# Kernel optimization log

Measured on AMD Instinct MI355X. Metric: run time of the kernel, lower is better.

The kernel has to match this reference:

```python
import jax, jax.numpy as jnp
import numpy as np

B, C_IN, C_OUT, H, K = 256, 64, 128, 1039, 6  # batch, in_ch, out_ch, num_hexagons, max_neighbors


def _make_neighbors(rng, num_hex, max_n):
    # valid neighbor indices first, -1 padding at the end (matches torch init)
    nb = np.full((num_hex, max_n), -1, dtype=np.int64)
    counts = rng.integers(3, max_n + 1, size=num_hex)
    for i in range(num_hex):
        nb[i, :counts[i]] = rng.choice(num_hex, size=counts[i], replace=False)
    return nb


def setup_inputs() -> dict:
    key = jax.random.key(0)
    k1, k2, k3 = jax.random.split(key, 3)
    rng = np.random.default_rng(0)
    x = jax.random.normal(k1, (B, C_IN, H), dtype=jnp.float32)
    neighbors = jnp.asarray(_make_neighbors(rng, H, K))
    weight_center = jax.random.normal(k2, (C_OUT, C_IN), dtype=jnp.float32) / np.sqrt(C_IN)
    weight_neighbors = jax.random.normal(k3, (C_OUT, C_IN, K), dtype=jnp.float32) / np.sqrt(C_IN * K)
    bias = jnp.zeros((C_OUT,), dtype=jnp.float32)
    return {"x": x, "neighbors": neighbors, "weight_center": weight_center,
            "weight_neighbors": weight_neighbors, "bias": bias}


def reference(x, neighbors, weight_center, weight_neighbors, bias):
    # x: [B, C_in, H]; neighbors: [H, K] with -1 padding at the tail
    mask = (neighbors >= 0)                        # [H, K]
    safe_idx = jnp.where(mask, neighbors, 0)       # [H, K]
    # gather neighbor features and zero out padded slots: [B, C_in, H, K]
    neigh = x[:, :, safe_idx] * mask.astype(x.dtype)[None, None, :, :]
    center = jnp.einsum('bch,oc->boh', x, weight_center)
    neigh_contrib = jnp.einsum('bchk,ock->boh', neigh, weight_neighbors)
    total_valid = (mask.sum(axis=-1) + 1).astype(x.dtype)  # [H]
    out = (center + neigh_contrib) / total_valid[None, None, :] + bias[None, :, None]
    return out
```

## Files before the change

### kernel.cpp

```cpp
#include <hip/hip_runtime.h>

#define BATCH 256
#define CIN   64
#define COUT  128
#define HEX   1039
#define KNB   6
#define ZROW  HEX
#define TILEH 48
#define NTILE 22
#define LDSB  ((HEX + 1) * 128)

typedef __attribute__((ext_vector_type(8))) short bf16x8;
typedef __attribute__((ext_vector_type(4))) float f32x4;

__device__ __forceinline__ unsigned short f2bf(float f) {
    unsigned int u = __builtin_bit_cast(unsigned int, f);
    u += 0x7fffu + ((u >> 16) & 1);
    return (unsigned short)(u >> 16);
}

__global__ __launch_bounds__(256) void k_prep(const float* __restrict__ wc,
                                              const float* __restrict__ wn,
                                              unsigned short* __restrict__ wf) {
    int e    = blockIdx.x * 256 + threadIdx.x;
    int j    = e & 7;
    int lane = (e >> 3) & 63;
    int mt   = (e >> 9) & 7;
    int kb   = e >> 12;
    int o  = mt * 16 + (lane & 15);
    int kd = kb * 32 + (lane >> 4) * 8 + j;
    int jn = kd >> 6;
    int c  = kd & 63;
    float v = (jn == 0) ? wc[o * CIN + c]
                        : wn[(o * CIN + c) * KNB + (jn - 1)];
    wf[e] = f2bf(v);
}

__global__ __launch_bounds__(768) void k_main(const float* __restrict__ x,
                                              const int* __restrict__ nb,
                                              const unsigned short* __restrict__ wf,
                                              const float* __restrict__ bias,
                                              float* __restrict__ out) {
    extern __shared__ __align__(16) unsigned short XT[];

    int b    = blockIdx.x;
    int tid  = threadIdx.x;
    int lane = tid & 63;
    int wv   = tid >> 6;
    int quad = lane >> 4;
    int l16  = lane & 15;
    int m    = wv & 3;
    int hq   = wv >> 2;

    const bf16x8* wfv = (const bf16x8*)wf;
    bf16x8 A[14][2];
    #pragma unroll
    for (int kb = 0; kb < 14; ++kb)
        #pragma unroll
        for (int mi = 0; mi < 2; ++mi)
            A[kb][mi] = wfv[(kb * 8 + 2 * m + mi) * 64 + lane];

    float bs[2][4];
    #pragma unroll
    for (int mi = 0; mi < 2; ++mi)
        #pragma unroll
        for (int r = 0; r < 4; ++r)
            bs[mi][r] = bias[(2 * m + mi) * 16 + quad * 4 + r];

    {
        const float* xb = x + (size_t)b * (CIN * HEX);
        #pragma unroll 1
        for (int t = 0; t < 11; ++t) {
            int e = t * 768 + tid;
            if (e < 8320) {
                int h  = e >> 3;
                int cc = e & 7;
                bf16x8 v = {};
                if (h < HEX) {
                    #pragma unroll
                    for (int k = 0; k < 8; ++k)
                        v[k] = (short)f2bf(xb[(size_t)(cc * 8 + k) * HEX + h]);
                }
                *(bf16x8*)((char*)XT + h * 128 + ((cc ^ (h & 7)) << 4)) = v;
            }
        }
    }
    __syncthreads();

    int ho = hq * 16 + l16;
    int rawn[6];
    int voff[7];

    auto loadraw = [&](int ht2) {
        int h  = ht2 * TILEH + ho;
        int hs = (h < HEX) ? h : 0;
        #pragma unroll
        for (int j = 0; j < KNB; ++j)
            rawn[j] = nb[hs * KNB + j];
    };
    auto offg = [&](int g) { return (g << 7) | ((quad ^ (g & 7)) << 4); };

    loadraw(0);
    float* outb = out + (size_t)b * ((size_t)COUT * HEX);

    #pragma unroll 1
    for (int ht = 0; ht < NTILE; ++ht) {
        int h  = ht * TILEH + ho;
        bool hv = (h < HEX);
        voff[0] = offg(hv ? h : ZROW);
        int cnt = 1;
        #pragma unroll
        for (int j = 0; j < KNB; ++j) {
            int t2 = rawn[j];
            bool val = hv && (t2 >= 0);
            cnt += val ? 1 : 0;
            voff[j + 1] = offg(val ? t2 : ZROW);
        }
        float inv = 1.0f / (float)cnt;
        if (ht + 1 < NTILE) loadraw(ht + 1);

        f32x4 acc[2] = {};
        #pragma unroll
        for (int ks = 0; ks < 14; ++ks) {
            int jn = ks >> 1;
            int xr = (ks & 1) << 6;
            bf16x8 bb = *(const bf16x8*)((const char*)XT + (voff[jn] ^ xr));
            acc[0] = __builtin_amdgcn_mfma_f32_16x16x32_bf16(A[ks][0], bb, acc[0], 0, 0, 0);
            acc[1] = __builtin_amdgcn_mfma_f32_16x16x32_bf16(A[ks][1], bb, acc[1], 0, 0, 0);
        }

        if (hv) {
            #pragma unroll
            for (int mi = 0; mi < 2; ++mi)
                #pragma unroll
                for (int r = 0; r < 4; ++r) {
                    int o = (2 * m + mi) * 16 + quad * 4 + r;
                    outb[(size_t)o * HEX + h] = acc[mi][r] * inv + bs[mi][r];
                }
        }
    }
}

extern "C" void kernel_launch(void* const* d_in, const int* in_sizes, int n_in,
                              void* d_out, int out_size, void* d_ws, size_t ws_size,
                              hipStream_t stream) {
    const float* x    = (const float*)d_in[0];
    const int*   nb   = (const int*)d_in[1];
    const float* wc   = (const float*)d_in[2];
    const float* wn   = (const float*)d_in[3];
    const float* bias = (const float*)d_in[4];
    float*       out  = (float*)d_out;

    unsigned short* wf = (unsigned short*)d_ws;

    static bool s_attr_done = false;
    if (!s_attr_done) {
        hipFuncSetAttribute((const void*)k_main,
                            hipFuncAttributeMaxDynamicSharedMemorySize, LDSB);
        s_attr_done = true;
    }

    hipLaunchKernelGGL(k_prep, dim3(224),   dim3(256), 0,    stream, wc, wn, wf);
    hipLaunchKernelGGL(k_main, dim3(BATCH), dim3(768), LDSB, stream,
                       x, nb, wf, bias, out);
}
```

Before: 221.3 us.

## Software-pipeline neighbor index loads and reload weights per tile from global

Restructures the main loop into a two-tile unrolled pipeline. Neighbor indices are prefetched two tiles ahead and LDS offsets are built one tile ahead, and all 14 B-fragments are issued from LDS before the MFMA chain. The 28 register-resident weight fragments are dropped; weights are now re-read from global/L2 inside every MFMA step, and launch bounds ask for 3 waves per SIMD. This trades register pressure for extra global weight traffic on each tile, hoping to hide latency better.

```diff
diff --git a/kernel.cpp b/kernel.cpp
--- a/kernel.cpp
+++ b/kernel.cpp
@@ -36,11 +36,65 @@
     wf[e] = f2bf(v);
 }
 
-__global__ __launch_bounds__(768) void k_main(const float* __restrict__ x,
-                                              const int* __restrict__ nb,
-                                              const unsigned short* __restrict__ wf,
-                                              const float* __restrict__ bias,
-                                              float* __restrict__ out) {
+
+#define LOADRAW(HT2, R)                                              \
+    if ((HT2) < NTILE) {                                             \
+        int h2_ = (HT2) * TILEH + ho;                                \
+        int hs_ = (h2_ < HEX) ? h2_ : 0;                             \
+        _Pragma("unroll")                                            \
+        for (int j = 0; j < KNB; ++j) R[j] = nb[hs_ * KNB + j];      \
+    }
+
+#define MAKEVOFF(T, R, V, INV)                                       \
+    if ((T) < NTILE) {                                               \
+        int h2_ = (T) * TILEH + ho;                                  \
+        bool hv_ = (h2_ < HEX);                                      \
+        V[0] = offg(hv_ ? h2_ : ZROW);                               \
+        int cnt_ = 1;                                                \
+        _Pragma("unroll")                                            \
+        for (int j = 0; j < KNB; ++j) {                              \
+            int t2_ = R[j];                                          \
+            bool val_ = hv_ && (t2_ >= 0);                           \
+            cnt_ += val_ ? 1 : 0;                                    \
+            V[j + 1] = offg(val_ ? t2_ : ZROW);                      \
+        }                                                            \
+        INV = 1.0f / (float)cnt_;                                    \
+    }
+
+#define TILE_STEP(HT, V, INV, RN, VN, INVN, RL)                      \
+    {                                                                \
+        bf16x8 bb[14];                                               \
+        _Pragma("unroll")                                            \
+        for (int ks = 0; ks < 14; ++ks)                              \
+            bb[ks] = *(const bf16x8*)((const char*)XT +              \
+                        (V[ks >> 1] ^ ((ks & 1) << 6)));             \
+        MAKEVOFF((HT) + 1, RN, VN, INVN);                            \
+        LOADRAW((HT) + 2, RL);                                       \
+        f32x4 acc0 = {}, acc1 = {};                                  \
+        _Pragma("unroll")                                            \
+        for (int ks = 0; ks < 14; ++ks) {                            \
+            acc0 = __builtin_amdgcn_mfma_f32_16x16x32_bf16(          \
+                wfv[(ks * 8 + 2 * m + 0) * 64 + lane], bb[ks], acc0, 0, 0, 0); \
+            acc1 = __builtin_amdgcn_mfma_f32_16x16x32_bf16(          \
+                wfv[(ks * 8 + 2 * m + 1) * 64 + lane], bb[ks], acc1, 0, 0, 0); \
+        }                                                            \
+        int he_ = (HT) * TILEH + ho;                                 \
+        if (he_ < HEX) {                                             \
+            _Pragma("unroll")                                        \
+            for (int r = 0; r < 4; ++r) {                            \
+                int o0_ = (2 * m + 0) * 16 + quad * 4 + r;           \
+                outb[(size_t)o0_ * HEX + he_] = acc0[r] * (INV) + bs[0][r]; \
+                int o1_ = (2 * m + 1) * 16 + quad * 4 + r;           \
+                outb[(size_t)o1_ * HEX + he_] = acc1[r] * (INV) + bs[1][r]; \
+            }                                                        \
+        }                                                            \
+    }
+
+__global__ __launch_bounds__(768, 3) void k_main(const float* __restrict__ x,
+                                                 const int* __restrict__ nb,
+                                                 const unsigned short* __restrict__ wf,
+                                                 const float* __restrict__ bias,
+                                                 float* __restrict__ out) {
     extern __shared__ __align__(16) unsigned short XT[];
 
     int b    = blockIdx.x;
@@ -53,12 +107,6 @@
     int hq   = wv >> 2;
 
     const bf16x8* wfv = (const bf16x8*)wf;
-    bf16x8 A[14][2];
-    #pragma unroll
-    for (int kb = 0; kb < 14; ++kb)
-        #pragma unroll
-        for (int mi = 0; mi < 2; ++mi)
-            A[kb][mi] = wfv[(kb * 8 + 2 * m + mi) * 64 + lane];
 
     float bs[2][4];
     #pragma unroll
@@ -88,56 +136,23 @@
     __syncthreads();
 
     int ho = hq * 16 + l16;
-    int rawn[6];
-    int voff[7];
-
-    auto loadraw = [&](int ht2) {
-        int h  = ht2 * TILEH + ho;
-        int hs = (h < HEX) ? h : 0;
-        #pragma unroll
-        for (int j = 0; j < KNB; ++j)
-            rawn[j] = nb[hs * KNB + j];
-    };
     auto offg = [&](int g) { return (g << 7) | ((quad ^ (g & 7)) << 4); };
 
-    loadraw(0);
     float* outb = out + (size_t)b * ((size_t)COUT * HEX);
 
+    int rawnA[6], rawnB[6];
+    int voffC[7], voffN[7];
+    float invC = 1.0f, invN = 1.0f;
+
+    LOADRAW(0, rawnA);
+    MAKEVOFF(0, rawnA, voffC, invC);
+    LOADRAW(1, rawnB);
+
     #pragma unroll 1
-    for (int ht = 0; ht < NTILE; ++ht) {
-        int h  = ht * TILEH + ho;
-        bool hv = (h < HEX);
-        voff[0] = offg(hv ? h : ZROW);
-        int cnt = 1;
-        #pragma unroll
-        for (int j = 0; j < KNB; ++j) {
-            int t2 = rawn[j];
-            bool val = hv && (t2 >= 0);
-            cnt += val ? 1 : 0;
-            voff[j + 1] = offg(val ? t2 : ZROW);
-        }
-        float inv = 1.0f / (float)cnt;
-        if (ht + 1 < NTILE) loadraw(ht + 1);
-
-        f32x4 acc[2] = {};
-        #pragma unroll
-        for (int ks = 0; ks < 14; ++ks) {
-            int jn = ks >> 1;
-            int xr = (ks & 1) << 6;
-            bf16x8 bb = *(const bf16x8*)((const char*)XT + (voff[jn] ^ xr));
-            acc[0] = __builtin_amdgcn_mfma_f32_16x16x32_bf16(A[ks][0], bb, acc[0], 0, 0, 0);
-            acc[1] = __builtin_amdgcn_mfma_f32_16x16x32_bf16(A[ks][1], bb, acc[1], 0, 0, 0);
-        }
-
-        if (hv) {
-            #pragma unroll
-            for (int mi = 0; mi < 2; ++mi)
-                #pragma unroll
-                for (int r = 0; r < 4; ++r) {
-                    int o = (2 * m + mi) * 16 + quad * 4 + r;
-                    outb[(size_t)o * HEX + h] = acc[mi][r] * inv + bs[mi][r];
-                }
-        }
+    for (int i = 0; i < NTILE / 2; ++i) {
+        int ht = 2 * i;
+        TILE_STEP(ht,     voffC, invC, rawnB, voffN, invN, rawnA);
+        TILE_STEP(ht + 1, voffN, invN, rawnA, voffC, invC, rawnB);
     }
 }
 
```

Result: slower. 387.9 us (+75.3%).
